# Optimization experiments

Hardware: AMD Instinct MI355X
Metric: run time of the kernel (lower is better)

Reference implementation:

```python
import jax, jax.numpy as jnp
import numpy as np

P = 16            # decode steps == n_process
M = 4             # number of physical nodes
CAPACITY = [4, 4, 4, 4]
B = 4096          # batch
S = 16            # n_process (sequence length)
G = 128           # gnn_dim
E = 256           # n_embed
H = 512           # n_hidden
CLIP = 10.0       # clip_logits
MASK_PENALTY = 1e8


def setup_inputs() -> dict:
    key = jax.random.key(0)
    ks = jax.random.split(key, 16)
    u = lambda k, shape: jax.random.uniform(k, shape, jnp.float32, -0.08, 0.08)
    return {
        "x": jax.random.normal(ks[0], (B, S, G), jnp.float32),
        "emb_W": u(ks[1], (E, G)),                 # embedding Linear (no bias)
        "enc_Wih": u(ks[2], (4 * H, E)),           # encoder LSTM (gate order i,f,g,o)
        "enc_Whh": u(ks[3], (4 * H, H)),
        "enc_b": u(ks[4], (4 * H,)),               # b_ih + b_hh folded into one bias
        "dec_Wih": u(ks[5], (4 * H, E)),           # decoder LSTM
        "dec_Whh": u(ks[6], (4 * H, H)),
        "dec_b": u(ks[7], (4 * H,)),
        "Wq2": u(ks[8], (H, H)),                   # pointer W_q2
        "bq2": u(ks[9], (H,)),
        "Wref2": u(ks[10], (H, H)),                # pointer W_ref2 (conv1d k=1 == linear)
        "bref2": u(ks[11], (H,)),
        "Vec2": u(ks[12], (H,)),
        "dec_input0": u(ks[13], (E,)),             # learned initial decoder input
    }


def lstm_cell(x, h, c, Wih, Whh, b):
    g = x @ Wih.T + h @ Whh.T + b
    i, f, gg, o = jnp.split(g, 4, axis=-1)
    c = jax.nn.sigmoid(f) * c + jax.nn.sigmoid(i) * jnp.tanh(gg)
    h = jax.nn.sigmoid(o) * jnp.tanh(c)
    return h, c


def reference(x, emb_W, enc_Wih, enc_Whh, enc_b, dec_Wih, dec_Whh, dec_b,
              Wq2, bq2, Wref2, bref2, Vec2, dec_input0):
    Bx, Sx, _ = x.shape
    emb = x @ emb_W.T                                  # (B,S,E)

    # ---- encoder LSTM over the sequence ----
    def enc_step(carry, xt):
        h, c = carry
        h, c = lstm_cell(xt, h, c, enc_Wih, enc_Whh, enc_b)
        return (h, c), h

    h0 = jnp.zeros((Bx, H), emb.dtype)
    (h, c), enc_hs = jax.lax.scan(enc_step, (h0, h0), jnp.swapaxes(emb, 0, 1))
    ref = jnp.swapaxes(enc_hs, 0, 1)                   # (B,S,H)

    # W_ref2 conv1d(k=1) applied to ref is step-invariant: hoist out of the loop
    u2 = jnp.einsum('bsh,oh->bso', ref, Wref2) + bref2  # (B,S,H)

    dec0 = jnp.broadcast_to(dec_input0, (Bx, E))
    mask0 = jnp.zeros((Bx, Sx), emb.dtype)

    def dec_step(carry, _):
        h, c, din, mask = carry
        h, c = lstm_cell(din, h, c, dec_Wih, dec_Whh, dec_b)
        qp = h @ Wq2.T + bq2                           # (B,H)
        t = CLIP * jnp.tanh(qp[:, None, :] + u2)       # (B,S,H)
        logits = jnp.einsum('h,bsh->bs', Vec2, t) - MASK_PENALTY * mask
        log_p = jax.nn.log_softmax(logits, axis=-1)    # (B,S)
        nxt = jnp.argmax(log_p, axis=1)                # greedy node selector
        din = jnp.take_along_axis(emb, nxt[:, None, None], axis=1)[:, 0, :]
        mask = mask + jax.nn.one_hot(nxt, Sx, dtype=mask.dtype)
        return (h, c, din, mask), (nxt, log_p)

    _, (pis, log_ps) = jax.lax.scan(dec_step, (h, c, dec0, mask0), None, length=P)
    pi = jnp.swapaxes(pis, 0, 1)                       # (B,P)
    log_ps = jnp.swapaxes(log_ps, 0, 1)                # (B,P,S)

    # log-likelihood of the chosen tour
    ll = jnp.take_along_axis(log_ps, pi[:, :, None], axis=2)[..., 0].sum(axis=1)

    # __get_mapping: node id per step depends only on the capacity vector
    nodes = jnp.asarray(np.repeat(np.arange(M), np.asarray(CAPACITY))[:P], jnp.int32)
    rows = jnp.arange(Bx)
    mapping = jnp.full((Bx, P), -1, jnp.int32)
    mapping = mapping.at[rows[:, None], pi].set(jnp.broadcast_to(nodes, (Bx, P)))
    return mapping, ll
```

## Files before the change

kernel.cpp:

```cpp
#include <hip/hip_runtime.h>
#include <cstddef>

#define Bsz  4096
#define Sseq 16
#define Gdim 128
#define Edim 256
#define Hdim 512
#define H4   2048
#define Psteps 16
#define BK   16

typedef short bfrag8 __attribute__((ext_vector_type(8)));
typedef float f32x4  __attribute__((ext_vector_type(4)));

__device__ __forceinline__ void split3(float f, unsigned short& h,
                                       unsigned short& m, unsigned short& l) {
    unsigned u = __float_as_uint(f);
    h = (unsigned short)(u >> 16);
    float r1 = f - __uint_as_float(u & 0xffff0000u);
    unsigned u1 = __float_as_uint(r1);
    m = (unsigned short)(u1 >> 16);
    float r2 = r1 - __uint_as_float(u1 & 0xffff0000u);
    l = (unsigned short)(__float_as_uint(r2) >> 16);
}

__global__ void fold_kernel(const float* __restrict__ encWih,
                            const float* __restrict__ encWhh,
                            const float* __restrict__ enc_b,
                            const float* __restrict__ decWih,
                            const float* __restrict__ decWhh,
                            const float* __restrict__ dec_b,
                            const float* __restrict__ embW,
                            const float* __restrict__ dec0,
                            unsigned short* __restrict__ encEh,
                            unsigned short* __restrict__ encEm,
                            unsigned short* __restrict__ encEl,
                            unsigned short* __restrict__ encWh,
                            unsigned short* __restrict__ encWm,
                            unsigned short* __restrict__ encWl,
                            unsigned short* __restrict__ decEh,
                            unsigned short* __restrict__ decEm,
                            unsigned short* __restrict__ decEl,
                            unsigned short* __restrict__ decWh,
                            unsigned short* __restrict__ decWm,
                            unsigned short* __restrict__ decWl,
                            float* __restrict__ encBI, float* __restrict__ decBI,
                            float* __restrict__ v0bI) {
    __shared__ float rE[Edim], rD[Edim];
    const int o = blockIdx.x;
    const int gate = o >> 9, j = o & 511;
    const int c = j * 4 + gate;
    const int g = threadIdx.x;
    rE[g]        = encWih[(size_t)o * Edim + g];
    rE[g + Gdim] = encWih[(size_t)o * Edim + g + Gdim];
    rD[g]        = decWih[(size_t)o * Edim + g];
    rD[g + Gdim] = decWih[(size_t)o * Edim + g + Gdim];
    __syncthreads();

    float se = 0.f, sd = 0.f;
#pragma unroll 8
    for (int e = 0; e < Edim; ++e) {
        float w = embW[e * Gdim + g];
        se += rE[e] * w;
        sd += rD[e] * w;
    }
    unsigned short h, m, l;
    split3(se, h, m, l);
    encEh[(size_t)c * Gdim + g] = h; encEm[(size_t)c * Gdim + g] = m;
    encEl[(size_t)c * Gdim + g] = l;
    split3(sd, h, m, l);
    decEh[(size_t)c * Gdim + g] = h; decEm[(size_t)c * Gdim + g] = m;
    decEl[(size_t)c * Gdim + g] = l;
    for (int k = g; k < Hdim; k += Gdim) {
        split3(encWhh[(size_t)o * Hdim + k], h, m, l);
        encWh[(size_t)c * Hdim + k] = h; encWm[(size_t)c * Hdim + k] = m;
        encWl[(size_t)c * Hdim + k] = l;
        split3(decWhh[(size_t)o * Hdim + k], h, m, l);
        decWh[(size_t)c * Hdim + k] = h; decWm[(size_t)c * Hdim + k] = m;
        decWl[(size_t)c * Hdim + k] = l;
    }
    if (g == 0) {
        encBI[c] = enc_b[o];
        decBI[c] = dec_b[o];
        float s = dec_b[o];
        for (int e = 0; e < Edim; ++e) s += rD[e] * dec0[e];
        v0bI[c] = s;
    }
}

__global__ __launch_bounds__(256) void fold_proj(
    const float* __restrict__ Wr, const float* __restrict__ Wq,
    unsigned short* __restrict__ rWh, unsigned short* __restrict__ rWm,
    unsigned short* __restrict__ rWl,
    unsigned short* __restrict__ qWh, unsigned short* __restrict__ qWm,
    unsigned short* __restrict__ qWl) {
    const int o = blockIdx.x;
    const float* src = blockIdx.y ? Wq : Wr;
    unsigned short* ph = blockIdx.y ? qWh : rWh;
    unsigned short* pm = blockIdx.y ? qWm : rWm;
    unsigned short* pl = blockIdx.y ? qWl : rWl;
    for (int k = threadIdx.x; k < Hdim; k += 256) {
        unsigned short h, m, l;
        split3(src[(size_t)o * Hdim + k], h, m, l);
        ph[(size_t)o * Hdim + k] = h;
        pm[(size_t)o * Hdim + k] = m;
        pl[(size_t)o * Hdim + k] = l;
    }
}

__global__ __launch_bounds__(256) void gates_mfma(
    const unsigned short* __restrict__ Wh1, const unsigned short* __restrict__ Wm1,
    const unsigned short* __restrict__ Wl1, int K1,
    const float* __restrict__ X, int ldx,
    const int* __restrict__ gather, int gmul,
    const unsigned short* __restrict__ Wh2, const unsigned short* __restrict__ Wm2,
    const unsigned short* __restrict__ Wl2, int K2,
    const float* __restrict__ Hin,
    const float* __restrict__ biasI,
    const float* __restrict__ c_in, float* __restrict__ h_out,
    float* __restrict__ c_out, int czero)
{
    __shared__ __align__(16) unsigned short wlds[2][3 * 4096];
    __shared__ __align__(16) float alds[2][128 * 32];

    const int tid = threadIdx.x;
    const int wv = tid >> 6, lane = tid & 63;
    const int lm = lane & 15, quad = lane >> 4;
    const int c0 = blockIdx.y * 128;
    const int mB0 = blockIdx.x * 128;

    int mrow[2];
#pragma unroll
    for (int tm = 0; tm < 2; ++tm) mrow[tm] = mB0 + wv * 32 + tm * 16 + lm;

    int srow[2], sqs[2];
#pragma unroll
    for (int i = 0; i < 2; ++i) {
        const int seg = i * 4 + wv;
        const int r = seg * 16 + (lane >> 2);
        srow[i] = r;
        sqs[i] = (lane & 3) ^ ((r >> 1) & 3);
    }
    size_t roff1[2], roff2[2];
#pragma unroll
    for (int i = 0; i < 2; ++i) {
        roff1[i] = (size_t)(c0 + srow[i]) * K1 + (size_t)(sqs[i] * 8);
        roff2[i] = (size_t)(c0 + srow[i]) * K2 + (size_t)(sqs[i] * 8);
    }

    const int asw = ((lane & 7) ^ (lane >> 3)) * 4;
    const float* asrcX[4];
    const float* asrcH[4];
#pragma unroll
    for (int i = 0; i < 4; ++i) {
        const int r = (wv * 4 + i) * 8 + (lane >> 3);
        const int m = mB0 + r;
        if (X) {
            size_t off = (size_t)m * ldx;
            if (gather) off += (size_t)gather[m] * gmul;
            asrcX[i] = X + off + asw;
        }
        if (Hin) asrcH[i] = Hin + (size_t)m * K2 + asw;
    }

    int boffW[8];
#pragma unroll
    for (int tn = 0; tn < 8; ++tn) {
        const int r = tn * 16 + lm;
        boffW[tn] = r * 32 + ((quad ^ ((r >> 1) & 3)) * 8);
    }
    int boffA1[2], boffA2[2];
#pragma unroll
    for (int tm = 0; tm < 2; ++tm) {
        const int r = wv * 32 + tm * 16 + lm;
        boffA1[tm] = r * 32 + (((2 * quad)     ^ (lm & 7)) << 2);
        boffA2[tm] = r * 32 + (((2 * quad + 1) ^ (lm & 7)) << 2);
    }

    auto stage = [&](int kcN, int buf) {
        const bool nX = kcN < K1;
        const int kb = nX ? kcN : kcN - K1;
#pragma unroll
        for (int i = 0; i < 2; ++i) {
            const int seg = i * 4 + wv;
            unsigned short* lb = &wlds[buf][seg * 512];
            const unsigned short* gh = (nX ? Wh1 + roff1[i] : Wh2 + roff2[i]) + kb;
            const unsigned short* gm = (nX ? Wm1 + roff1[i] : Wm2 + roff2[i]) + kb;
            const unsigned short* gl = (nX ? Wl1 + roff1[i] : Wl2 + roff2[i]) + kb;
            __builtin_amdgcn_global_load_lds(
                (const __attribute__((address_space(1))) void*)gh,
                (__attribute__((address_space(3))) void*)(lb), 16, 0, 0);
            __builtin_amdgcn_global_load_lds(
                (const __attribute__((address_space(1))) void*)gm,
                (__attribute__((address_space(3))) void*)(lb + 4096), 16, 0, 0);
            __builtin_amdgcn_global_load_lds(
                (const __attribute__((address_space(1))) void*)gl,
                (__attribute__((address_space(3))) void*)(lb + 8192), 16, 0, 0);
        }
#pragma unroll
        for (int i = 0; i < 4; ++i) {
            float* lb = &alds[buf][(wv * 4 + i) * 256];
            const float* src = (nX ? asrcX[i] : asrcH[i]) + kb;
            __builtin_amdgcn_global_load_lds(
                (const __attribute__((address_space(1))) void*)src,
                (__attribute__((address_space(3))) void*)lb, 16, 0, 0);
        }
    };

    f32x4 acc[8][2];
#pragma unroll
    for (int i = 0; i < 8; ++i)
#pragma unroll
        for (int j = 0; j < 2; ++j) acc[i][j] = (f32x4){0.f, 0.f, 0.f, 0.f};

    const int KT = K1 + K2;
    stage(0, 0);
    int cur = 0;

    for (int kc = 0; kc < KT; kc += 32) {
        __syncthreads();
        if (kc + 32 < KT) stage(kc + 32, cur ^ 1);

        const float* abuf = alds[cur];
        bfrag8 bh[2], bm[2], bl[2];
#pragma unroll
        for (int tm = 0; tm < 2; ++tm) {
            float a8[8];
            *(float4*)&a8[0] = *(const float4*)(abuf + boffA1[tm]);
            *(float4*)&a8[4] = *(const float4*)(abuf + boffA2[tm]);
#pragma unroll
            for (int j = 0; j < 8; ++j) {
                unsigned short h, m, l;
                split3(a8[j], h, m, l);
                bh[tm][j] = (short)h; bm[tm][j] = (short)m; bl[tm][j] = (short)l;
            }
        }

        const unsigned short* bufp = wlds[cur];
#pragma unroll
        for (int hh = 0; hh < 2; ++hh) {
            bfrag8 ah[4], am4[4], al[4];
#pragma unroll
            for (int t = 0; t < 4; ++t) {
                const int tn = hh * 4 + t;
                ah[t]  = *(const bfrag8*)(bufp + boffW[tn]);
                am4[t] = *(const bfrag8*)(bufp + 4096 + boffW[tn]);
                al[t]  = *(const bfrag8*)(bufp + 8192 + boffW[tn]);
            }
#pragma unroll
            for (int tm = 0; tm < 2; ++tm) {
#pragma unroll
                for (int t = 0; t < 4; ++t) {
                    const int tn = hh * 4 + t;
                    f32x4 c = acc[tn][tm];
                    c = __builtin_amdgcn_mfma_f32_16x16x32_bf16(ah[t], bl[tm], c, 0, 0, 0);
                    c = __builtin_amdgcn_mfma_f32_16x16x32_bf16(al[t], bh[tm], c, 0, 0, 0);
                    c = __builtin_amdgcn_mfma_f32_16x16x32_bf16(am4[t], bm[tm], c, 0, 0, 0);
                    c = __builtin_amdgcn_mfma_f32_16x16x32_bf16(ah[t], bm[tm], c, 0, 0, 0);
                    c = __builtin_amdgcn_mfma_f32_16x16x32_bf16(am4[t], bh[tm], c, 0, 0, 0);
                    c = __builtin_amdgcn_mfma_f32_16x16x32_bf16(ah[t], bh[tm], c, 0, 0, 0);
                    acc[tn][tm] = c;
                }
            }
        }
        cur ^= 1;
    }

#pragma unroll
    for (int tn = 0; tn < 8; ++tn) {
        const int nb = c0 + tn * 16 + quad * 4;
        float4 bb = *(const float4*)(biasI + nb);
        const int j = nb >> 2;
#pragma unroll
        for (int tm = 0; tm < 2; ++tm) {
            const size_t idx = (size_t)mrow[tm] * Hdim + j;
            float gi = acc[tn][tm][0] + bb.x;
            float gf = acc[tn][tm][1] + bb.y;
            float gg = acc[tn][tm][2] + bb.z;
            float go = acc[tn][tm][3] + bb.w;
            float si = 1.f / (1.f + expf(-gi));
            float sf = 1.f / (1.f + expf(-gf));
            float so = 1.f / (1.f + expf(-go));
            float co = czero ? 0.f : c_in[idx];
            float cn = si * tanhf(gg) + sf * co;
            c_out[idx] = cn;
            h_out[idx] = so * tanhf(cn);
        }
    }
}

__global__ __launch_bounds__(256) void proj_mfma(
    const unsigned short* __restrict__ Wh, const unsigned short* __restrict__ Wm,
    const unsigned short* __restrict__ Wl,
    const float* __restrict__ A,
    const float* __restrict__ bias,
    float* __restrict__ C, int ldc)
{
    __shared__ __align__(16) unsigned short wlds[2][3 * 2048];
    __shared__ __align__(16) float alds[2][64 * 32];

    const int tid = threadIdx.x;
    const int wv = tid >> 6, lane = tid & 63;
    const int lm = lane & 15, quad = lane >> 4;
    const int nB0 = blockIdx.y * 64;
    const int mB0 = blockIdx.x * 64;

    const int rw = tid >> 2;
    const int sqw = (tid & 3) ^ ((rw >> 1) & 3);
    const size_t wroff = (size_t)(nB0 + rw) * Hdim + (size_t)(sqw * 8);

    const int asw = ((lane & 7) ^ (lane >> 3)) * 4;
    const float* asrc[2];
#pragma unroll
    for (int i = 0; i < 2; ++i) {
        const int r = i * 32 + wv * 8 + (lane >> 3);
        asrc[i] = A + (size_t)(mB0 + r) * Hdim + asw;
    }

    int boffW[4];
#pragma unroll
    for (int tn = 0; tn < 4; ++tn) {
        const int r = tn * 16 + lm;
        boffW[tn] = r * 32 + ((quad ^ ((r >> 1) & 3)) * 8);
    }
    const int ra = wv * 16 + lm;
    const int boffA1 = ra * 32 + (((2 * quad)     ^ (lm & 7)) << 2);
    const int boffA2 = ra * 32 + (((2 * quad + 1) ^ (lm & 7)) << 2);

    auto stage = [&](int kb, int buf) {
        unsigned short* lb0 = &wlds[buf][wv * 512];
        __builtin_amdgcn_global_load_lds(
            (const __attribute__((address_space(1))) void*)(Wh + wroff + kb),
            (__attribute__((address_space(3))) void*)(lb0), 16, 0, 0);
        __builtin_amdgcn_global_load_lds(
            (const __attribute__((address_space(1))) void*)(Wm + wroff + kb),
            (__attribute__((address_space(3))) void*)(lb0 + 2048), 16, 0, 0);
        __builtin_amdgcn_global_load_lds(
            (const __attribute__((address_space(1))) void*)(Wl + wroff + kb),
            (__attribute__((address_space(3))) void*)(lb0 + 4096), 16, 0, 0);
#pragma unroll
        for (int i = 0; i < 2; ++i) {
            float* lb = &alds[buf][(i * 32 + wv * 8) * 32];
            __builtin_amdgcn_global_load_lds(
                (const __attribute__((address_space(1))) void*)(asrc[i] + kb),
                (__attribute__((address_space(3))) void*)lb, 16, 0, 0);
        }
    };

    f32x4 acc[4];
#pragma unroll
    for (int i = 0; i < 4; ++i) acc[i] = (f32x4){0.f, 0.f, 0.f, 0.f};

    stage(0, 0);
    int cur = 0;

    for (int kc = 0; kc < Hdim; kc += 32) {
        __syncthreads();
        if (kc + 32 < Hdim) stage(kc + 32, cur ^ 1);

        const float* abuf = alds[cur];
        float a8[8];
        *(float4*)&a8[0] = *(const float4*)(abuf + boffA1);
        *(float4*)&a8[4] = *(const float4*)(abuf + boffA2);
        bfrag8 bh, bm, bl;
#pragma unroll
        for (int j = 0; j < 8; ++j) {
            unsigned short h, m, l;
            split3(a8[j], h, m, l);
            bh[j] = (short)h; bm[j] = (short)m; bl[j] = (short)l;
        }

        const unsigned short* bufp = wlds[cur];
#pragma unroll
        for (int tn = 0; tn < 4; ++tn) {
            bfrag8 ah  = *(const bfrag8*)(bufp + boffW[tn]);
            bfrag8 am4 = *(const bfrag8*)(bufp + 2048 + boffW[tn]);
            bfrag8 al  = *(const bfrag8*)(bufp + 4096 + boffW[tn]);
            f32x4 c = acc[tn];
            c = __builtin_amdgcn_mfma_f32_16x16x32_bf16(ah,  bl, c, 0, 0, 0);
            c = __builtin_amdgcn_mfma_f32_16x16x32_bf16(al,  bh, c, 0, 0, 0);
            c = __builtin_amdgcn_mfma_f32_16x16x32_bf16(am4, bm, c, 0, 0, 0);
            c = __builtin_amdgcn_mfma_f32_16x16x32_bf16(ah,  bm, c, 0, 0, 0);
            c = __builtin_amdgcn_mfma_f32_16x16x32_bf16(am4, bh, c, 0, 0, 0);
            c = __builtin_amdgcn_mfma_f32_16x16x32_bf16(ah,  bh, c, 0, 0, 0);
            acc[tn] = c;
        }
        cur ^= 1;
    }

    const int m = mB0 + wv * 16 + lm;
#pragma unroll
    for (int tn = 0; tn < 4; ++tn) {
        const int n = nB0 + tn * 16 + quad * 4;
        float4 bb = *(const float4*)(bias + n);
        float4 o;
        o.x = acc[tn][0] + bb.x;
        o.y = acc[tn][1] + bb.y;
        o.z = acc[tn][2] + bb.z;
        o.w = acc[tn][3] + bb.w;
        *(float4*)(C + (size_t)m * ldc + n) = o;
    }
}

__global__ __launch_bounds__(256) void attn_step(const float* __restrict__ qp,
                                                 const float* __restrict__ u2,
                                                 const float* __restrict__ Vec2,
                                                 float* __restrict__ mask,
                                                 float* __restrict__ ll_ws,
                                                 int* __restrict__ nxt,
                                                 float* __restrict__ out_map,
                                                 float* __restrict__ out_ll,
                                                 int step, int node) {
    const int b = blockIdx.x;
    __shared__ float qpS[Hdim];
    __shared__ float vS[Hdim];
    __shared__ float logitS[Sseq];
    const int tid = threadIdx.x;
    qpS[tid]       = qp[(size_t)b * Hdim + tid];
    qpS[tid + 256] = qp[(size_t)b * Hdim + 256 + tid];
    vS[tid]        = Vec2[tid];
    vS[tid + 256]  = Vec2[256 + tid];
    __syncthreads();

    const int wave = tid >> 6, lane = tid & 63;
    for (int si = 0; si < 4; ++si) {
        int s = wave * 4 + si;
        const float* u2p = u2 + ((size_t)b * Sseq + s) * Hdim;
        float sum = 0.f;
#pragma unroll
        for (int i = 0; i < 8; ++i) {
            int hh = lane + i * 64;
            sum += vS[hh] * tanhf(qpS[hh] + u2p[hh]);
        }
        for (int off = 32; off > 0; off >>= 1) sum += __shfl_down(sum, off);
        if (lane == 0) {
            float pen = step ? mask[b * Sseq + s] * 1e8f : 0.f;
            logitS[s] = 10.f * sum - pen;
        }
    }
    __syncthreads();

    if (tid == 0) {
        float mx = logitS[0];
        int am = 0;
        for (int s = 1; s < Sseq; ++s)
            if (logitS[s] > mx) { mx = logitS[s]; am = s; }
        float se = 0.f;
        for (int s = 0; s < Sseq; ++s) se += expf(logitS[s] - mx);
        float lp = -logf(se);
        float llv = (step ? ll_ws[b] : 0.f) + lp;
        ll_ws[b] = llv;
        out_ll[b] = llv;
        nxt[b] = am;
        if (step == 0) {
            for (int s = 0; s < Sseq; ++s) mask[b * Sseq + s] = (s == am) ? 1.f : 0.f;
        } else {
            mask[b * Sseq + am] += 1.f;
        }
        out_map[b * Sseq + am] = (float)node;
    }
}

extern "C" void kernel_launch(void* const* d_in, const int* in_sizes, int n_in,
                              void* d_out, int out_size, void* d_ws, size_t ws_size,
                              hipStream_t stream) {
    const float* x       = (const float*)d_in[0];
    const float* emb_W   = (const float*)d_in[1];
    const float* enc_Wih = (const float*)d_in[2];
    const float* enc_Whh = (const float*)d_in[3];
    const float* enc_b   = (const float*)d_in[4];
    const float* dec_Wih = (const float*)d_in[5];
    const float* dec_Whh = (const float*)d_in[6];
    const float* dec_b   = (const float*)d_in[7];
    const float* Wq2     = (const float*)d_in[8];
    const float* bq2     = (const float*)d_in[9];
    const float* Wref2   = (const float*)d_in[10];
    const float* bref2   = (const float*)d_in[11];
    const float* Vec2    = (const float*)d_in[12];
    const float* dec0    = (const float*)d_in[13];

    float* ws      = (float*)d_ws;
    float* u2      = ws;
    float* h0      = u2 + (size_t)Bsz * Sseq * Hdim;
    float* c0      = h0 + (size_t)Bsz * Hdim;
    float* h1      = c0 + (size_t)Bsz * Hdim;
    float* c1      = h1 + (size_t)Bsz * Hdim;
    float* qp      = c1 + (size_t)Bsz * Hdim;
    float* mask    = qp + (size_t)Bsz * Hdim;
    float* ll      = mask + (size_t)Bsz * Sseq;
    int*   nxt     = (int*)(ll + Bsz);
    float* encBI   = (float*)(nxt + Bsz);
    float* decBI   = encBI + H4;
    float* v0bI    = decBI + H4;
    unsigned short* us = (unsigned short*)(v0bI + H4);
    unsigned short* encEh = us;                       us += (size_t)H4 * Gdim;
    unsigned short* encEm = us;                       us += (size_t)H4 * Gdim;
    unsigned short* encEl = us;                       us += (size_t)H4 * Gdim;
    unsigned short* encWh = us;                       us += (size_t)H4 * Hdim;
    unsigned short* encWm = us;                       us += (size_t)H4 * Hdim;
    unsigned short* encWl = us;                       us += (size_t)H4 * Hdim;
    unsigned short* decEh = us;                       us += (size_t)H4 * Gdim;
    unsigned short* decEm = us;                       us += (size_t)H4 * Gdim;
    unsigned short* decEl = us;                       us += (size_t)H4 * Gdim;
    unsigned short* decWh = us;                       us += (size_t)H4 * Hdim;
    unsigned short* decWm = us;                       us += (size_t)H4 * Hdim;
    unsigned short* decWl = us;                       us += (size_t)H4 * Hdim;
    unsigned short* prWh = us;                        us += (size_t)Hdim * Hdim;
    unsigned short* prWm = us;                        us += (size_t)Hdim * Hdim;
    unsigned short* prWl = us;                        us += (size_t)Hdim * Hdim;
    unsigned short* pqWh = us;                        us += (size_t)Hdim * Hdim;
    unsigned short* pqWm = us;                        us += (size_t)Hdim * Hdim;
    unsigned short* pqWl = us;                        us += (size_t)Hdim * Hdim;

    float* out_map = (float*)d_out;
    float* out_ll  = out_map + (size_t)Bsz * Psteps;

    static const int nodes[Psteps] = {0,0,0,0, 1,1,1,1, 2,2,2,2, 3,3,3,3};

    fold_kernel<<<H4, Gdim, 0, stream>>>(enc_Wih, enc_Whh, enc_b,
                                         dec_Wih, dec_Whh, dec_b,
                                         emb_W, dec0,
                                         encEh, encEm, encEl, encWh, encWm, encWl,
                                         decEh, decEm, decEl, decWh, decWm, decWl,
                                         encBI, decBI, v0bI);
    fold_proj<<<dim3(Hdim, 2), 256, 0, stream>>>(Wref2, Wq2,
                                                 prWh, prWm, prWl,
                                                 pqWh, pqWm, pqWl);

    const dim3 gBig(32, 16);
    const dim3 gPr(64, 8);

    for (int t = 0; t < Sseq; ++t) {
        float* ho = (t & 1) ? h0 : h1;
        float* co = (t & 1) ? c0 : c1;
        const float* hi = (t & 1) ? h1 : h0;
        const float* ci = (t & 1) ? c1 : c0;
        if (t == 0) {
            gates_mfma<<<gBig, 256, 0, stream>>>(
                encEh, encEm, encEl, Gdim,
                x, Sseq * Gdim, nullptr, 0,
                nullptr, nullptr, nullptr, 0, nullptr,
                encBI, ci, ho, co, 1);
        } else {
            gates_mfma<<<gBig, 256, 0, stream>>>(
                encEh, encEm, encEl, Gdim,
                x + t * Gdim, Sseq * Gdim, nullptr, 0,
                encWh, encWm, encWl, Hdim, hi,
                encBI, ci, ho, co, 0);
        }
        proj_mfma<<<gPr, 256, 0, stream>>>(prWh, prWm, prWl, ho, bref2,
                                           u2 + (size_t)t * Hdim, Sseq * Hdim);
    }

    for (int p = 0; p < Psteps; ++p) {
        const int u = Sseq + p;
        float* ho = (u & 1) ? h0 : h1;
        float* co = (u & 1) ? c0 : c1;
        const float* hi = (u & 1) ? h1 : h0;
        const float* ci = (u & 1) ? c1 : c0;
        if (p == 0) {
            gates_mfma<<<gBig, 256, 0, stream>>>(
                nullptr, nullptr, nullptr, 0,
                nullptr, 0, nullptr, 0,
                decWh, decWm, decWl, Hdim, hi,
                v0bI, ci, ho, co, 0);
        } else {
            gates_mfma<<<gBig, 256, 0, stream>>>(
                decEh, decEm, decEl, Gdim,
                x, Sseq * Gdim, nxt, Gdim,
                decWh, decWm, decWl, Hdim, hi,
                decBI, ci, ho, co, 0);
        }
        proj_mfma<<<gPr, 256, 0, stream>>>(pqWh, pqWm, pqWl, ho, bq2,
                                           qp, Hdim);
        attn_step<<<Bsz, 256, 0, stream>>>(qp, u2, Vec2, mask, ll, nxt,
                                           out_map, out_ll, p, nodes[p]);
    }
}
```

Measured before the change: 3.252 ms.

## Shrink gates tile to 64 rows and load activations straight from global

The LSTM gates kernel now gives each wave 16 batch rows instead of 32, so a block covers 64 batch rows and the grid doubles along the batch axis. Activation fragments are read directly from global memory into registers each k-step instead of being staged through an LDS buffer. This removes the activation LDS staging and its shared memory, and halves the accumulators, which should raise occupancy. In exchange, each loaded weight tile is reused over half as many rows, so total weight traffic doubles, and the global activation loads are less coalesced and are not prefetched.

```diff
diff --git a/kernel.cpp b/kernel.cpp
--- a/kernel.cpp
+++ b/kernel.cpp
@@ -121,17 +121,14 @@
     float* __restrict__ c_out, int czero)
 {
     __shared__ __align__(16) unsigned short wlds[2][3 * 4096];
-    __shared__ __align__(16) float alds[2][128 * 32];
 
     const int tid = threadIdx.x;
     const int wv = tid >> 6, lane = tid & 63;
     const int lm = lane & 15, quad = lane >> 4;
     const int c0 = blockIdx.y * 128;
-    const int mB0 = blockIdx.x * 128;
-
-    int mrow[2];
-#pragma unroll
-    for (int tm = 0; tm < 2; ++tm) mrow[tm] = mB0 + wv * 32 + tm * 16 + lm;
+    const int mB0 = blockIdx.x * 64;
+
+    const int mrow = mB0 + wv * 16 + lm;
 
     int srow[2], sqs[2];
 #pragma unroll
@@ -148,33 +145,20 @@
         roff2[i] = (size_t)(c0 + srow[i]) * K2 + (size_t)(sqs[i] * 8);
     }
 
-    const int asw = ((lane & 7) ^ (lane >> 3)) * 4;
-    const float* asrcX[4];
-    const float* asrcH[4];
-#pragma unroll
-    for (int i = 0; i < 4; ++i) {
-        const int r = (wv * 4 + i) * 8 + (lane >> 3);
-        const int m = mB0 + r;
-        if (X) {
-            size_t off = (size_t)m * ldx;
-            if (gather) off += (size_t)gather[m] * gmul;
-            asrcX[i] = X + off + asw;
-        }
-        if (Hin) asrcH[i] = Hin + (size_t)m * K2 + asw;
-    }
+    const float* xr = nullptr;
+    const float* hr = nullptr;
+    if (X) {
+        size_t off = (size_t)mrow * ldx;
+        if (gather) off += (size_t)gather[mrow] * gmul;
+        xr = X + off;
+    }
+    if (Hin) hr = Hin + (size_t)mrow * K2;
 
     int boffW[8];
 #pragma unroll
     for (int tn = 0; tn < 8; ++tn) {
         const int r = tn * 16 + lm;
         boffW[tn] = r * 32 + ((quad ^ ((r >> 1) & 3)) * 8);
-    }
-    int boffA1[2], boffA2[2];
-#pragma unroll
-    for (int tm = 0; tm < 2; ++tm) {
-        const int r = wv * 32 + tm * 16 + lm;
-        boffA1[tm] = r * 32 + (((2 * quad)     ^ (lm & 7)) << 2);
-        boffA2[tm] = r * 32 + (((2 * quad + 1) ^ (lm & 7)) << 2);
     }
 
     auto stage = [&](int kcN, int buf) {
@@ -197,21 +181,11 @@
                 (const __attribute__((address_space(1))) void*)gl,
                 (__attribute__((address_space(3))) void*)(lb + 8192), 16, 0, 0);
         }
-#pragma unroll
-        for (int i = 0; i < 4; ++i) {
-            float* lb = &alds[buf][(wv * 4 + i) * 256];
-            const float* src = (nX ? asrcX[i] : asrcH[i]) + kb;
-            __builtin_amdgcn_global_load_lds(
-                (const __attribute__((address_space(1))) void*)src,
-                (__attribute__((address_space(3))) void*)lb, 16, 0, 0);
-        }
     };
 
-    f32x4 acc[8][2];
-#pragma unroll
-    for (int i = 0; i < 8; ++i)
-#pragma unroll
-        for (int j = 0; j < 2; ++j) acc[i][j] = (f32x4){0.f, 0.f, 0.f, 0.f};
+    f32x4 acc[8];
+#pragma unroll
+    for (int i = 0; i < 8; ++i) acc[i] = (f32x4){0.f, 0.f, 0.f, 0.f};
 
     const int KT = K1 + K2;
     stage(0, 0);
@@ -221,19 +195,19 @@
         __syncthreads();
         if (kc + 32 < KT) stage(kc + 32, cur ^ 1);
 
-        const float* abuf = alds[cur];
-        bfrag8 bh[2], bm[2], bl[2];
-#pragma unroll
-        for (int tm = 0; tm < 2; ++tm) {
-            float a8[8];
-            *(float4*)&a8[0] = *(const float4*)(abuf + boffA1[tm]);
-            *(float4*)&a8[4] = *(const float4*)(abuf + boffA2[tm]);
-#pragma unroll
-            for (int j = 0; j < 8; ++j) {
-                unsigned short h, m, l;
-                split3(a8[j], h, m, l);
-                bh[tm][j] = (short)h; bm[tm][j] = (short)m; bl[tm][j] = (short)l;
-            }
+        const bool inX = kc < K1;
+        const int kk = (inX ? kc : kc - K1) + quad * 8;
+
+        const float* p = (inX ? xr : hr) + kk;
+        float a8[8];
+        *(float4*)&a8[0] = *(const float4*)(p);
+        *(float4*)&a8[4] = *(const float4*)(p + 4);
+        bfrag8 bh, bm, bl;
+#pragma unroll
+        for (int j = 0; j < 8; ++j) {
+            unsigned short h, m, l;
+            split3(a8[j], h, m, l);
+            bh[j] = (short)h; bm[j] = (short)m; bl[j] = (short)l;
         }
 
         const unsigned short* bufp = wlds[cur];
@@ -248,19 +222,16 @@
                 al[t]  = *(const bfrag8*)(bufp + 8192 + boffW[tn]);
             }
 #pragma unroll
-            for (int tm = 0; tm < 2; ++tm) {
-#pragma unroll
-                for (int t = 0; t < 4; ++t) {
-                    const int tn = hh * 4 + t;
-                    f32x4 c = acc[tn][tm];
-                    c = __builtin_amdgcn_mfma_f32_16x16x32_bf16(ah[t], bl[tm], c, 0, 0, 0);
-                    c = __builtin_amdgcn_mfma_f32_16x16x32_bf16(al[t], bh[tm], c, 0, 0, 0);
-                    c = __builtin_amdgcn_mfma_f32_16x16x32_bf16(am4[t], bm[tm], c, 0, 0, 0);
-                    c = __builtin_amdgcn_mfma_f32_16x16x32_bf16(ah[t], bm[tm], c, 0, 0, 0);
-                    c = __builtin_amdgcn_mfma_f32_16x16x32_bf16(am4[t], bh[tm], c, 0, 0, 0);
-                    c = __builtin_amdgcn_mfma_f32_16x16x32_bf16(ah[t], bh[tm], c, 0, 0, 0);
-                    acc[tn][tm] = c;
-                }
+            for (int t = 0; t < 4; ++t) {
+                const int tn = hh * 4 + t;
+                f32x4 c = acc[tn];
+                c = __builtin_amdgcn_mfma_f32_16x16x32_bf16(ah[t], bl, c, 0, 0, 0);
+                c = __builtin_amdgcn_mfma_f32_16x16x32_bf16(al[t], bh, c, 0, 0, 0);
+                c = __builtin_amdgcn_mfma_f32_16x16x32_bf16(am4[t], bm, c, 0, 0, 0);
+                c = __builtin_amdgcn_mfma_f32_16x16x32_bf16(ah[t], bm, c, 0, 0, 0);
+                c = __builtin_amdgcn_mfma_f32_16x16x32_bf16(am4[t], bh, c, 0, 0, 0);
+                c = __builtin_amdgcn_mfma_f32_16x16x32_bf16(ah[t], bh, c, 0, 0, 0);
+                acc[tn] = c;
             }
         }
         cur ^= 1;
@@ -271,21 +242,18 @@
         const int nb = c0 + tn * 16 + quad * 4;
         float4 bb = *(const float4*)(biasI + nb);
         const int j = nb >> 2;
-#pragma unroll
-        for (int tm = 0; tm < 2; ++tm) {
-            const size_t idx = (size_t)mrow[tm] * Hdim + j;
-            float gi = acc[tn][tm][0] + bb.x;
-            float gf = acc[tn][tm][1] + bb.y;
-            float gg = acc[tn][tm][2] + bb.z;
-            float go = acc[tn][tm][3] + bb.w;
-            float si = 1.f / (1.f + expf(-gi));
-            float sf = 1.f / (1.f + expf(-gf));
-            float so = 1.f / (1.f + expf(-go));
-            float co = czero ? 0.f : c_in[idx];
-            float cn = si * tanhf(gg) + sf * co;
-            c_out[idx] = cn;
-            h_out[idx] = so * tanhf(cn);
-        }
+        const size_t idx = (size_t)mrow * Hdim + j;
+        float gi = acc[tn][0] + bb.x;
+        float gf = acc[tn][1] + bb.y;
+        float gg = acc[tn][2] + bb.z;
+        float go = acc[tn][3] + bb.w;
+        float si = 1.f / (1.f + expf(-gi));
+        float sf = 1.f / (1.f + expf(-gf));
+        float so = 1.f / (1.f + expf(-go));
+        float co = czero ? 0.f : c_in[idx];
+        float cn = si * tanhf(gg) + sf * co;
+        c_out[idx] = cn;
+        h_out[idx] = so * tanhf(cn);
     }
 }
 
@@ -527,7 +495,7 @@
                                                  prWh, prWm, prWl,
                                                  pqWh, pqWm, pqWl);
 
-    const dim3 gBig(32, 16);
+    const dim3 gBig(64, 16);
     const dim3 gPr(64, 8);
 
     for (int t = 0; t < Sseq; ++t) {
```

After: 3.836 ms. 1.18x slower.
